# Kernel optimization log

Hardware: AMD Instinct MI355X
Metric: run time of the kernel (lower is better)

## Reference

```python
import jax, jax.numpy as jnp
import numpy as np


def setup_inputs() -> dict:
    key = jax.random.key(0)
    k1, k2, k3 = jax.random.split(key, 3)
    B, L, H, E = 2, 2048, 16, 64
    queries = jax.random.normal(k1, (B, L, H, E), dtype=jnp.float32)
    keys = jax.random.normal(k2, (B, L, H, E), dtype=jnp.float32)
    values = jax.random.normal(k3, (B, L, H, E), dtype=jnp.float32)
    a1 = jnp.ones((), dtype=jnp.float32)
    a2 = jnp.ones((), dtype=jnp.float32)
    return {"queries": queries, "keys": keys, "values": values, "a1": a1, "a2": a2}


def reference(queries, keys, values, a1, a2):
    # ASSAAttention forward (eval mode: dropout is identity)
    B, L, H, E = queries.shape
    scale = 1.0 / jnp.sqrt(jnp.asarray(E, queries.dtype))
    # shared QK scores: [B, H, L, S]
    qk_scores = jnp.einsum('blhe,bshe->bhls', queries, keys) * scale
    # sparse path: squared-ReLU weighting
    ssa_scores = jax.nn.relu(qk_scores) ** 2
    ssa_output = jnp.einsum('bhls,bshd->blhd', ssa_scores, values)
    # dense path: softmax weighting
    dsa_scores = jax.nn.softmax(qk_scores, axis=-1)
    dsa_output = jnp.einsum('bhls,bshd->blhd', dsa_scores, values)
    # scalar blend with softmax over (a1, a2)
    w1 = jnp.exp(a1)
    w2 = jnp.exp(a2)
    alpha1 = w1 / (w1 + w2)
    alpha2 = w2 / (w1 + w2)
    return alpha1 * ssa_output + alpha2 * dsa_output
```

## Files before the change

### kernel.cpp

```cpp
#include <hip/hip_runtime.h>
#include <hip/hip_bf16.h>

typedef __attribute__((ext_vector_type(8))) short short8;
typedef __attribute__((ext_vector_type(4))) short short4v;
typedef __attribute__((ext_vector_type(4))) float f32x4;
typedef __attribute__((ext_vector_type(4))) unsigned uint4v;

#define LOG2E 1.4426950408889634f
#define ILN2SQ 0.4804530139182014f

__device__ __forceinline__ unsigned packbf2(float a, float b) {
  __hip_bfloat162 h = __float22bfloat162_rn(make_float2(a, b));
  return *reinterpret_cast<unsigned*>(&h);
}
__device__ __forceinline__ int swz(int row) {
  return ((row & 7) << 4) ^ (((row >> 3) & 3) << 5);
}
__device__ __forceinline__ void gload16(const void* g, void* l) {
  __builtin_amdgcn_global_load_lds(
      (const __attribute__((address_space(1))) unsigned int*)g,
      (__attribute__((address_space(3))) unsigned int*)l, 16, 0, 0);
}

__global__ __launch_bounds__(256) void assa_prep(
    const float* __restrict__ K, const float* __restrict__ V, char* __restrict__ WS)
{
  constexpr int L = 2048, RS = 1024, E = 64;
  char* KP = WS;
  char* VTP = WS + (size_t)8 * 1024 * 1024;
  __shared__ float tile[64][65];
  const int tid = threadIdx.x;

  if (blockIdx.x < 1024) {
    const int gid = blockIdx.x * 256 + tid;
    const int rid = gid >> 2;
    const int e0 = (gid & 3) * 16;
    const int bh = rid >> 11, s = rid & 2047;
    const int b = bh >> 4, h = bh & 15;
    const float* kr = K + ((size_t)b * L + s) * RS + h * E + e0;
    const float4 u0 = *(const float4*)(kr);
    const float4 u1 = *(const float4*)(kr + 4);
    const float4 u2 = *(const float4*)(kr + 8);
    const float4 u3 = *(const float4*)(kr + 12);
    uint4v w0, w1;
    w0[0] = packbf2(u0.x, u0.y); w0[1] = packbf2(u0.z, u0.w);
    w0[2] = packbf2(u1.x, u1.y); w0[3] = packbf2(u1.z, u1.w);
    w1[0] = packbf2(u2.x, u2.y); w1[1] = packbf2(u2.z, u2.w);
    w1[2] = packbf2(u3.x, u3.y); w1[3] = packbf2(u3.z, u3.w);
    char* dst = KP + (size_t)rid * 128;
    const int sz = swz(s);
    *(uint4v*)(dst + ((e0 * 2) ^ sz)) = w0;
    *(uint4v*)(dst + ((e0 * 2 + 16) ^ sz)) = w1;
  } else {
    const int bx = blockIdx.x - 1024;
    const int bh = bx >> 5, t5 = bx & 31;
    const int b = bh >> 4, h = bh & 15;
    const float* vb = V + ((size_t)b * L + t5 * 64) * RS + h * E;
    {
      const int key = tid >> 2, e0 = (tid & 3) * 16;
      const float* vr = vb + (size_t)key * RS + e0;
      const float4 u0 = *(const float4*)(vr);
      const float4 u1 = *(const float4*)(vr + 4);
      const float4 u2 = *(const float4*)(vr + 8);
      const float4 u3 = *(const float4*)(vr + 12);
      float* tr = &tile[key][e0];
      tr[0] = u0.x; tr[1] = u0.y; tr[2] = u0.z; tr[3] = u0.w;
      tr[4] = u1.x; tr[5] = u1.y; tr[6] = u1.z; tr[7] = u1.w;
      tr[8] = u2.x; tr[9] = u2.y; tr[10] = u2.z; tr[11] = u2.w;
      tr[12] = u3.x; tr[13] = u3.y; tr[14] = u3.z; tr[15] = u3.w;
    }
    __syncthreads();
    const int e = tid >> 2, p0 = (tid & 3) * 16;
    const int gg = p0 >> 4;
    uint4v w0, w1;
    #pragma unroll
    for (int i = 0; i < 4; ++i) {
      const int pa = 2 * i, pb = 2 * i + 1;
      const int k_a = ((pa >> 2) & 3) * 16 + gg * 4 + (pa & 3);
      const int k_b = ((pb >> 2) & 3) * 16 + gg * 4 + (pb & 3);
      w0[i] = packbf2(tile[k_a][e], tile[k_b][e]);
    }
    #pragma unroll
    for (int i = 0; i < 4; ++i) {
      const int pa = 8 + 2 * i, pb = 9 + 2 * i;
      const int k_a = ((pa >> 2) & 3) * 16 + gg * 4 + (pa & 3);
      const int k_b = ((pb >> 2) & 3) * 16 + gg * 4 + (pb & 3);
      w1[i] = packbf2(tile[k_a][e], tile[k_b][e]);
    }
    char* dst = VTP + ((size_t)bx * 64 + e) * 128;
    const int sz = swz(e);
    *(uint4v*)(dst + ((p0 * 2) ^ sz)) = w0;
    *(uint4v*)(dst + ((p0 * 2 + 16) ^ sz)) = w1;
  }
}

__global__ __launch_bounds__(256, 2) void assa_fused(
    const float* __restrict__ Q, const char* __restrict__ WS,
    const float* __restrict__ A1, const float* __restrict__ A2,
    float* __restrict__ O)
{
  constexpr int L = 2048, H = 16, E = 64, RS = H * E;

  __shared__ __align__(16) char Kb[2 * 8192];
  __shared__ __align__(16) char Vb[2 * 8192];

  const int t = threadIdx.x;
  const int wv = t >> 6;
  const int lane = t & 63;
  const int g = lane >> 4;
  const int c = lane & 15;

  const int bh = blockIdx.x;
  const int q0 = blockIdx.y * 128;
  const int b = bh >> 4;
  const int h = bh & 15;

  const float* qb = Q + (size_t)b * L * RS + (size_t)h * E;
  float* ob = O + (size_t)b * L * RS + (size_t)h * E;
  const char* KP = WS;
  const char* VTP = WS + (size_t)8 * 1024 * 1024;

  const float a1 = A1[0], a2 = A2[0];
  const float am = fmaxf(a1, a2);
  const float e1 = expf(a1 - am), e2 = expf(a2 - am);
  const float alpha1 = (e1 / (e1 + e2)) * ILN2SQ;
  const float alpha2 = e2 / (e1 + e2);

  short8 aqA[2], aqB[2];
  {
    const float qs = 0.125f * LOG2E;
    #pragma unroll
    for (int setb = 0; setb < 2; ++setb) {
      const float* qr = qb + (size_t)(q0 + wv * 32 + setb * 16 + c) * RS;
      #pragma unroll
      for (int ks = 0; ks < 2; ++ks) {
        const float4 u0 = *(const float4*)(qr + ks * 32 + g * 8);
        const float4 u1 = *(const float4*)(qr + ks * 32 + g * 8 + 4);
        unsigned p0 = packbf2(u0.x * qs, u0.y * qs);
        unsigned p1 = packbf2(u0.z * qs, u0.w * qs);
        unsigned p2 = packbf2(u1.x * qs, u1.y * qs);
        unsigned p3 = packbf2(u1.z * qs, u1.w * qs);
        short8 f;
        f[0] = (short)(p0 & 0xffff); f[1] = (short)(p0 >> 16);
        f[2] = (short)(p1 & 0xffff); f[3] = (short)(p1 >> 16);
        f[4] = (short)(p2 & 0xffff); f[5] = (short)(p2 >> 16);
        f[6] = (short)(p3 & 0xffff); f[7] = (short)(p3 >> 16);
        if (setb) aqB[ks] = f; else aqA[ks] = f;
      }
    }
  }

  int ka[8];
  #pragma unroll
  for (int kt = 0; kt < 4; ++kt) {
    const int row = kt * 16 + c;
    const int s = swz(row);
    ka[kt * 2 + 0] = (row * 128 + g * 16) ^ s;
    ka[kt * 2 + 1] = (row * 128 + 64 + g * 16) ^ s;
  }
  int va[8];
  #pragma unroll
  for (int et = 0; et < 4; ++et) {
    const int row = et * 16 + c;
    const int s = swz(row);
    va[et * 2 + 0] = (row * 128 + g * 32) ^ s;
    va[et * 2 + 1] = (row * 128 + g * 32 + 16) ^ s;
  }

  const f32x4 zero4 = {0.0f, 0.0f, 0.0f, 0.0f};
  f32x4 odA[4], osA[4], odB[4], osB[4];
  #pragma unroll
  for (int i = 0; i < 4; ++i) { odA[i] = zero4; osA[i] = zero4; odB[i] = zero4; osB[i] = zero4; }
  float psumA = 0.0f, psumB = 0.0f;

  const char* kp = KP + (size_t)bh * (2048 * 128) + wv * 1024 + lane * 16;
  const char* vp = VTP + (size_t)bh * (2048 * 128) + wv * 1024 + lane * 16;
  char* kd = Kb + wv * 1024;
  char* vd = Vb + wv * 1024;

#define STAGE(TOFF, HALF)                              \
  do {                                                 \
    gload16(kp + (TOFF), kd + (HALF));                 \
    gload16(kp + (TOFF) + 4096, kd + (HALF) + 4096);   \
    gload16(vp + (TOFF), vd + (HALF));                 \
    gload16(vp + (TOFF) + 4096, vd + (HALF) + 4096);   \
  } while (0)

#define PROC(ACC, OD, OS, PSUM)                                                      \
  do {                                                                               \
    _Pragma("unroll")                                                                \
    for (int kt = 0; kt < 4; ++kt) {                                                 \
      const float x0 = __builtin_amdgcn_exp2f(ACC[kt][0]);                           \
      const float x1 = __builtin_amdgcn_exp2f(ACC[kt][1]);                           \
      const float x2 = __builtin_amdgcn_exp2f(ACC[kt][2]);                           \
      const float x3 = __builtin_amdgcn_exp2f(ACC[kt][3]);                           \
      PSUM += (x0 + x1) + (x2 + x3);                                                 \
      const float r0 = fmaxf(ACC[kt][0], 0.0f), r1 = fmaxf(ACC[kt][1], 0.0f);        \
      const float r2 = fmaxf(ACC[kt][2], 0.0f), r3 = fmaxf(ACC[kt][3], 0.0f);        \
      union { unsigned u[2]; short4v v; } pdu, psu;                                  \
      pdu.u[0] = packbf2(x0, x1); pdu.u[1] = packbf2(x2, x3);                        \
      psu.u[0] = packbf2(r0 * r0, r1 * r1); psu.u[1] = packbf2(r2 * r2, r3 * r3);    \
      const short4v pd = pdu.v, ps = psu.v;                                          \
      _Pragma("unroll")                                                              \
      for (int et = 0; et < 4; ++et) {                                               \
        const short8 vsrc = (kt < 2) ? vv[et] : vw[et];                              \
        short4v vf;                                                                  \
        if (kt & 1) { vf[0] = vsrc[4]; vf[1] = vsrc[5]; vf[2] = vsrc[6]; vf[3] = vsrc[7]; } \
        else        { vf[0] = vsrc[0]; vf[1] = vsrc[1]; vf[2] = vsrc[2]; vf[3] = vsrc[3]; } \
        OD[et] = __builtin_amdgcn_mfma_f32_16x16x16bf16_1k(vf, pd, OD[et], 0, 0, 0); \
        OS[et] = __builtin_amdgcn_mfma_f32_16x16x16bf16_1k(vf, ps, OS[et], 0, 0, 0); \
      }                                                                              \
    }                                                                                \
  } while (0)

#define COMPUTE(OFS)                                                                 \
  do {                                                                               \
    f32x4 aA[4], aB[4];                                                              \
    _Pragma("unroll")                                                                \
    for (int i = 0; i < 4; ++i) { aA[i] = zero4; aB[i] = zero4; }                    \
    _Pragma("unroll")                                                                \
    for (int kt = 0; kt < 4; ++kt) {                                                 \
      const short8 kf0 = *(const short8*)(Kb + ka[kt * 2 + 0] + (OFS));              \
      const short8 kf1 = *(const short8*)(Kb + ka[kt * 2 + 1] + (OFS));              \
      aA[kt] = __builtin_amdgcn_mfma_f32_16x16x32_bf16(kf0, aqA[0], aA[kt], 0, 0, 0);\
      aA[kt] = __builtin_amdgcn_mfma_f32_16x16x32_bf16(kf1, aqA[1], aA[kt], 0, 0, 0);\
      aB[kt] = __builtin_amdgcn_mfma_f32_16x16x32_bf16(kf0, aqB[0], aB[kt], 0, 0, 0);\
      aB[kt] = __builtin_amdgcn_mfma_f32_16x16x32_bf16(kf1, aqB[1], aB[kt], 0, 0, 0);\
    }                                                                                \
    short8 vv[4], vw[4];                                                             \
    _Pragma("unroll")                                                                \
    for (int et = 0; et < 4; ++et) {                                                 \
      vv[et] = *(const short8*)(Vb + va[et * 2 + 0] + (OFS));                        \
      vw[et] = *(const short8*)(Vb + va[et * 2 + 1] + (OFS));                        \
    }                                                                                \
    PROC(aA, odA, osA, psumA);                                                       \
    PROC(aB, odB, osB, psumB);                                                       \
  } while (0)

  STAGE(0, 0);
  __syncthreads();
  size_t toff = 8192;
  for (int it = 0; it < 32; it += 2) {
    STAGE(toff, 8192); toff += 8192;
    COMPUTE(0);
    __syncthreads();
    if (it + 2 < 32) { STAGE(toff, 0); toff += 8192; }
    COMPUTE(8192);
    __syncthreads();
  }
#undef STAGE
#undef PROC
#undef COMPUTE

  float lA = psumA;
  lA += __shfl_xor(lA, 16);
  lA += __shfl_xor(lA, 32);
  float lB = psumB;
  lB += __shfl_xor(lB, 16);
  lB += __shfl_xor(lB, 32);

  const float wdA = alpha2 / lA;
  const float wdB = alpha2 / lB;
  float* orowA = ob + (size_t)(q0 + wv * 32 + c) * RS;
  float* orowB = orowA + (size_t)16 * RS;
  #pragma unroll
  for (int et = 0; et < 4; ++et) {
    float4 oa, obv;
    oa.x = alpha1 * osA[et][0] + wdA * odA[et][0];
    oa.y = alpha1 * osA[et][1] + wdA * odA[et][1];
    oa.z = alpha1 * osA[et][2] + wdA * odA[et][2];
    oa.w = alpha1 * osA[et][3] + wdA * odA[et][3];
    obv.x = alpha1 * osB[et][0] + wdB * odB[et][0];
    obv.y = alpha1 * osB[et][1] + wdB * odB[et][1];
    obv.z = alpha1 * osB[et][2] + wdB * odB[et][2];
    obv.w = alpha1 * osB[et][3] + wdB * odB[et][3];
    *(float4*)(orowA + et * 16 + g * 4) = oa;
    *(float4*)(orowB + et * 16 + g * 4) = obv;
  }
}

extern "C" void kernel_launch(void* const* d_in, const int* in_sizes, int n_in,
                              void* d_out, int out_size, void* d_ws, size_t ws_size,
                              hipStream_t stream) {
  const float* q = (const float*)d_in[0];
  const float* k = (const float*)d_in[1];
  const float* v = (const float*)d_in[2];
  const float* a1 = (const float*)d_in[3];
  const float* a2 = (const float*)d_in[4];
  float* out = (float*)d_out;
  char* ws = (char*)d_ws;

  assa_prep<<<2048, 256, 0, stream>>>(k, v, ws);
  dim3 grid(32, 16);
  assa_fused<<<grid, 256, 0, stream>>>(q, ws, a1, a2, out);
}
```

Baseline: 89.34 us.

## Use 16x16x32 bf16 MFMA for PV products with permuted V key layout

The PV stage now concatenates two kt tiles of P into a single 8-element operand and issues 16x16x32 MFMAs instead of pairs of 16x16x16 MFMAs. This halves the number of PV MFMA instructions and removes the per-element shuffling of V fragments. To keep the k-index mapping consistent, the prep kernel permutes the V-transpose key order through a new pv_key function, and the LDS read addresses change to match. The risk is that a wrong key permutation gives wrong results, and packing P for all tiles before use adds register pressure.

```diff
diff --git a/kernel.cpp b/kernel.cpp
--- a/kernel.cpp
+++ b/kernel.cpp
@@ -2,7 +2,6 @@
 #include <hip/hip_bf16.h>
 
 typedef __attribute__((ext_vector_type(8))) short short8;
-typedef __attribute__((ext_vector_type(4))) short short4v;
 typedef __attribute__((ext_vector_type(4))) float f32x4;
 typedef __attribute__((ext_vector_type(4))) unsigned uint4v;
 
@@ -20,6 +19,11 @@
   __builtin_amdgcn_global_load_lds(
       (const __attribute__((address_space(1))) unsigned int*)g,
       (__attribute__((address_space(3))) unsigned int*)l, 16, 0, 0);
+}
+
+__device__ __forceinline__ int pv_key(int p) {
+  const int R = p >> 5, g = (p & 31) >> 3, jj = p & 7;
+  return (R * 2 + (jj >> 2)) * 16 + g * 4 + (jj & 3);
 }
 
 __global__ __launch_bounds__(256) void assa_prep(
@@ -71,22 +75,13 @@
     }
     __syncthreads();
     const int e = tid >> 2, p0 = (tid & 3) * 16;
-    const int gg = p0 >> 4;
     uint4v w0, w1;
     #pragma unroll
-    for (int i = 0; i < 4; ++i) {
-      const int pa = 2 * i, pb = 2 * i + 1;
-      const int k_a = ((pa >> 2) & 3) * 16 + gg * 4 + (pa & 3);
-      const int k_b = ((pb >> 2) & 3) * 16 + gg * 4 + (pb & 3);
-      w0[i] = packbf2(tile[k_a][e], tile[k_b][e]);
-    }
+    for (int i = 0; i < 4; ++i)
+      w0[i] = packbf2(tile[pv_key(p0 + 2 * i)][e], tile[pv_key(p0 + 2 * i + 1)][e]);
     #pragma unroll
-    for (int i = 0; i < 4; ++i) {
-      const int pa = 8 + 2 * i, pb = 9 + 2 * i;
-      const int k_a = ((pa >> 2) & 3) * 16 + gg * 4 + (pa & 3);
-      const int k_b = ((pb >> 2) & 3) * 16 + gg * 4 + (pb & 3);
-      w1[i] = packbf2(tile[k_a][e], tile[k_b][e]);
-    }
+    for (int i = 0; i < 4; ++i)
+      w1[i] = packbf2(tile[pv_key(p0 + 8 + 2 * i)][e], tile[pv_key(p0 + 9 + 2 * i)][e]);
     char* dst = VTP + ((size_t)bx * 64 + e) * 128;
     const int sz = swz(e);
     *(uint4v*)(dst + ((p0 * 2) ^ sz)) = w0;
@@ -136,16 +131,12 @@
       for (int ks = 0; ks < 2; ++ks) {
         const float4 u0 = *(const float4*)(qr + ks * 32 + g * 8);
         const float4 u1 = *(const float4*)(qr + ks * 32 + g * 8 + 4);
-        unsigned p0 = packbf2(u0.x * qs, u0.y * qs);
-        unsigned p1 = packbf2(u0.z * qs, u0.w * qs);
-        unsigned p2 = packbf2(u1.x * qs, u1.y * qs);
-        unsigned p3 = packbf2(u1.z * qs, u1.w * qs);
-        short8 f;
-        f[0] = (short)(p0 & 0xffff); f[1] = (short)(p0 >> 16);
-        f[2] = (short)(p1 & 0xffff); f[3] = (short)(p1 >> 16);
-        f[4] = (short)(p2 & 0xffff); f[5] = (short)(p2 >> 16);
-        f[6] = (short)(p3 & 0xffff); f[7] = (short)(p3 >> 16);
-        if (setb) aqB[ks] = f; else aqA[ks] = f;
+        union { unsigned u[4]; short8 s; } f;
+        f.u[0] = packbf2(u0.x * qs, u0.y * qs);
+        f.u[1] = packbf2(u0.z * qs, u0.w * qs);
+        f.u[2] = packbf2(u1.x * qs, u1.y * qs);
+        f.u[3] = packbf2(u1.z * qs, u1.w * qs);
+        if (setb) aqB[ks] = f.s; else aqA[ks] = f.s;
       }
     }
   }
@@ -163,8 +154,8 @@
   for (int et = 0; et < 4; ++et) {
     const int row = et * 16 + c;
     const int s = swz(row);
-    va[et * 2 + 0] = (row * 128 + g * 32) ^ s;
-    va[et * 2 + 1] = (row * 128 + g * 32 + 16) ^ s;
+    va[et * 2 + 0] = (row * 128 + g * 16) ^ s;
+    va[et * 2 + 1] = (row * 128 + 64 + g * 16) ^ s;
   }
 
   const f32x4 zero4 = {0.0f, 0.0f, 0.0f, 0.0f};
@@ -177,6 +168,8 @@
   const char* vp = VTP + (size_t)bh * (2048 * 128) + wv * 1024 + lane * 16;
   char* kd = Kb + wv * 1024;
   char* vd = Vb + wv * 1024;
+
+  union U8 { unsigned u[4]; short8 s; };
 
 #define STAGE(TOFF, HALF)                              \
   do {                                                 \
@@ -188,6 +181,7 @@
 
 #define PROC(ACC, OD, OS, PSUM)                                                      \
   do {                                                                               \
+    unsigned pdw[8], psw[8];                                                         \
     _Pragma("unroll")                                                                \
     for (int kt = 0; kt < 4; ++kt) {                                                 \
       const float x0 = __builtin_amdgcn_exp2f(ACC[kt][0]);                           \
@@ -197,18 +191,23 @@
       PSUM += (x0 + x1) + (x2 + x3);                                                 \
       const float r0 = fmaxf(ACC[kt][0], 0.0f), r1 = fmaxf(ACC[kt][1], 0.0f);        \
       const float r2 = fmaxf(ACC[kt][2], 0.0f), r3 = fmaxf(ACC[kt][3], 0.0f);        \
-      union { unsigned u[2]; short4v v; } pdu, psu;                                  \
-      pdu.u[0] = packbf2(x0, x1); pdu.u[1] = packbf2(x2, x3);                        \
-      psu.u[0] = packbf2(r0 * r0, r1 * r1); psu.u[1] = packbf2(r2 * r2, r3 * r3);    \
-      const short4v pd = pdu.v, ps = psu.v;                                          \
+      pdw[kt * 2 + 0] = packbf2(x0, x1);                                             \
+      pdw[kt * 2 + 1] = packbf2(x2, x3);                                             \
+      psw[kt * 2 + 0] = packbf2(r0 * r0, r1 * r1);                                   \
+      psw[kt * 2 + 1] = packbf2(r2 * r2, r3 * r3);                                   \
+    }                                                                                \
+    _Pragma("unroll")                                                                \
+    for (int tp = 0; tp < 2; ++tp) {                                                 \
+      U8 bpd, bps;                                                                   \
+      bpd.u[0] = pdw[tp * 4 + 0]; bpd.u[1] = pdw[tp * 4 + 1];                        \
+      bpd.u[2] = pdw[tp * 4 + 2]; bpd.u[3] = pdw[tp * 4 + 3];                        \
+      bps.u[0] = psw[tp * 4 + 0]; bps.u[1] = psw[tp * 4 + 1];                        \
+      bps.u[2] = psw[tp * 4 + 2]; bps.u[3] = psw[tp * 4 + 3];                        \
       _Pragma("unroll")                                                              \
       for (int et = 0; et < 4; ++et) {                                               \
-        const short8 vsrc = (kt < 2) ? vv[et] : vw[et];                              \
-        short4v vf;                                                                  \
-        if (kt & 1) { vf[0] = vsrc[4]; vf[1] = vsrc[5]; vf[2] = vsrc[6]; vf[3] = vsrc[7]; } \
-        else        { vf[0] = vsrc[0]; vf[1] = vsrc[1]; vf[2] = vsrc[2]; vf[3] = vsrc[3]; } \
-        OD[et] = __builtin_amdgcn_mfma_f32_16x16x16bf16_1k(vf, pd, OD[et], 0, 0, 0); \
-        OS[et] = __builtin_amdgcn_mfma_f32_16x16x16bf16_1k(vf, ps, OS[et], 0, 0, 0); \
+        const short8 vf = tp ? vfr1[et] : vfr0[et];                                  \
+        OD[et] = __builtin_amdgcn_mfma_f32_16x16x32_bf16(vf, bpd.s, OD[et], 0, 0, 0);\
+        OS[et] = __builtin_amdgcn_mfma_f32_16x16x32_bf16(vf, bps.s, OS[et], 0, 0, 0);\
       }                                                                              \
     }                                                                                \
   } while (0)
@@ -227,11 +226,11 @@
       aB[kt] = __builtin_amdgcn_mfma_f32_16x16x32_bf16(kf0, aqB[0], aB[kt], 0, 0, 0);\
       aB[kt] = __builtin_amdgcn_mfma_f32_16x16x32_bf16(kf1, aqB[1], aB[kt], 0, 0, 0);\
     }                                                                                \
-    short8 vv[4], vw[4];                                                             \
+    short8 vfr0[4], vfr1[4];                                                         \
     _Pragma("unroll")                                                                \
     for (int et = 0; et < 4; ++et) {                                                 \
-      vv[et] = *(const short8*)(Vb + va[et * 2 + 0] + (OFS));                        \
-      vw[et] = *(const short8*)(Vb + va[et * 2 + 1] + (OFS));                        \
+      vfr0[et] = *(const short8*)(Vb + va[et * 2 + 0] + (OFS));                      \
+      vfr1[et] = *(const short8*)(Vb + va[et * 2 + 1] + (OFS));                      \
     }                                                                                \
     PROC(aA, odA, osA, psumA);                                                       \
     PROC(aB, odB, osB, psumB);                                                       \
```

Result: faster. 78.33 us (-12.3%).
